# Kernel tuning notes

Hardware: AMD Instinct MI355X
Metric: run time of the kernel (lower is better)

## Reference

```python
import jax, jax.numpy as jnp
import numpy as np

B, S, NI, NQK, NV = 8, 2048, 1024, 128, 128

def setup_inputs() -> dict:
    key = jax.random.key(0)
    ks = jax.random.split(key, 7)
    sc_i = 1.0 / np.sqrt(NI)
    x = jax.random.normal(ks[0], (B, S, NI), dtype=jnp.float32)
    Wq = jax.random.uniform(ks[1], (NQK, NI), dtype=jnp.float32, minval=-sc_i, maxval=sc_i)
    bq = jax.random.uniform(ks[2], (NQK,), dtype=jnp.float32, minval=-sc_i, maxval=sc_i)
    Wk = jax.random.uniform(ks[3], (NQK, NI), dtype=jnp.float32, minval=-sc_i, maxval=sc_i)
    bk = jax.random.uniform(ks[4], (NQK,), dtype=jnp.float32, minval=-sc_i, maxval=sc_i)
    Wv = jax.random.uniform(ks[5], (NV, NI), dtype=jnp.float32, minval=-sc_i, maxval=sc_i)
    bv = jax.random.uniform(ks[6], (NV,), dtype=jnp.float32, minval=-sc_i, maxval=sc_i)
    return {"x": x, "Wq": Wq, "bq": bq, "Wk": Wk, "bk": bk, "Wv": Wv, "bv": bv}

def reference(x, Wq, bq, Wk, bk, Wv, bv):
    # torch nn.Linear: y = x @ W.T + b
    q = jnp.einsum('bsi,di->bsd', x, Wq) + bq  # [B,S,NQK]
    k = jnp.einsum('bsi,di->bsd', x, Wk) + bk  # [B,S,NQK]
    v = jnp.einsum('bsi,di->bsd', x, Wv) + bv  # [B,S,NV]
    # NOTE: original has no 1/sqrt(d) scaling
    Z = jnp.einsum('bqd,bkd->bqk', q, k)       # [B,S,S]
    Z = jax.nn.softmax(Z, axis=2)
    y = jnp.einsum('bqk,bkd->bqd', Z, v)       # [B,S,NV]
    return y
```

## Files before the change

### kernel.cpp

```cpp
#include <hip/hip_runtime.h>
#include <hip/hip_bf16.h>
#include <cstdint>

#define B_ 8
#define S_ 2048
#define NI_ 1024
#define D_ 128
#define M_ (B_ * S_)

typedef __attribute__((ext_vector_type(8))) short bf16x8;
typedef __attribute__((ext_vector_type(8))) unsigned short u16x8;
typedef __attribute__((ext_vector_type(4))) float f32x4;

__device__ __forceinline__ unsigned short f2bf(float f) {
    union { float f; uint32_t u; } v; v.f = f;
    uint32_t u = v.u;
    u += 0x7fff + ((u >> 16) & 1);
    return (unsigned short)(u >> 16);
}

__device__ __forceinline__ void gload16(const void* g, void* l) {
    __builtin_amdgcn_global_load_lds((const __attribute__((address_space(1))) void*)g,
                                     (__attribute__((address_space(3))) void*)l, 16, 0, 0);
}

__global__ __launch_bounds__(256) void k_pack_w(const float* __restrict__ Wq, const float* __restrict__ bq,
                                                const float* __restrict__ Wk, const float* __restrict__ bk,
                                                const float* __restrict__ Wv, const float* __restrict__ bv,
                                                unsigned short* __restrict__ wb, float* __restrict__ bias) {
    int t = blockIdx.x * 256 + threadIdx.x;
    int e = t * 8;
    const float* src; int off;
    if (e < 131072)      { src = Wq; off = e; }
    else if (e < 262144) { src = Wk; off = e - 131072; }
    else                 { src = Wv; off = e - 262144; }
    float4 a = *(const float4*)(src + off);
    float4 b = *(const float4*)(src + off + 4);
    u16x8 r;
    r[0] = f2bf(a.x); r[1] = f2bf(a.y); r[2] = f2bf(a.z); r[3] = f2bf(a.w);
    r[4] = f2bf(b.x); r[5] = f2bf(b.y); r[6] = f2bf(b.z); r[7] = f2bf(b.w);
    *(u16x8*)(wb + e) = r;
    if (t < 384)
        bias[t] = (t < 128) ? bq[t] : (t < 256) ? bk[t - 128] : bv[t - 256];
}

__global__ __launch_bounds__(256) void k_qkv(const float* __restrict__ x,
                                             const unsigned short* __restrict__ wb,
                                             const float* __restrict__ bias,
                                             unsigned short* __restrict__ q,
                                             unsigned short* __restrict__ kout,
                                             unsigned short* __restrict__ vT) {
    __shared__ __align__(16) unsigned short As[128 * 32];
    __shared__ __align__(16) unsigned short Bs[128 * 32];
    const int tid = threadIdx.x;
    const int m0 = blockIdx.x * 128;
    const int n0 = blockIdx.y * 128;
    const int l = tid & 63, w = tid >> 6;
    const int wr = w >> 1, wc = w & 1;
    const int lr = l & 15, lg = l >> 4;
    const int sr = tid >> 2;
    const int sc = (tid & 3) * 8;

    f32x4 acc[4][4] = {};

    for (int k0 = 0; k0 < NI_; k0 += 32) {
        gload16(wb + (long)(n0 + sr) * NI_ + k0 + sc,        Bs + tid * 8);
        gload16(wb + (long)(n0 + 64 + sr) * NI_ + k0 + sc,   Bs + 2048 + tid * 8);
        const float* xg0 = x + (long)(m0 + sr) * NI_ + k0 + sc;
        const float* xg1 = x + (long)(m0 + 64 + sr) * NI_ + k0 + sc;
        float4 a0 = *(const float4*)xg0, a1 = *(const float4*)(xg0 + 4);
        float4 a2 = *(const float4*)xg1, a3 = *(const float4*)(xg1 + 4);
        union { __hip_bfloat162 h[4]; u16x8 v; } r0, r1;
        r0.h[0] = __float22bfloat162_rn(make_float2(a0.x, a0.y));
        r0.h[1] = __float22bfloat162_rn(make_float2(a0.z, a0.w));
        r0.h[2] = __float22bfloat162_rn(make_float2(a1.x, a1.y));
        r0.h[3] = __float22bfloat162_rn(make_float2(a1.z, a1.w));
        r1.h[0] = __float22bfloat162_rn(make_float2(a2.x, a2.y));
        r1.h[1] = __float22bfloat162_rn(make_float2(a2.z, a2.w));
        r1.h[2] = __float22bfloat162_rn(make_float2(a3.x, a3.y));
        r1.h[3] = __float22bfloat162_rn(make_float2(a3.z, a3.w));
        *(u16x8*)(As + tid * 8) = r0.v;
        *(u16x8*)(As + 2048 + tid * 8) = r1.v;
        __syncthreads();
        bf16x8 a[4], b[4];
#pragma unroll
        for (int i = 0; i < 4; i++)
            a[i] = *(const bf16x8*)(As + (wr * 64 + i * 16 + lr) * 32 + lg * 8);
#pragma unroll
        for (int j = 0; j < 4; j++)
            b[j] = *(const bf16x8*)(Bs + (wc * 64 + j * 16 + lr) * 32 + lg * 8);
#pragma unroll
        for (int i = 0; i < 4; i++)
#pragma unroll
            for (int j = 0; j < 4; j++)
                acc[i][j] = __builtin_amdgcn_mfma_f32_16x16x32_bf16(a[i], b[j], acc[i][j], 0, 0, 0);
        __syncthreads();
    }

#pragma unroll
    for (int i = 0; i < 4; i++)
#pragma unroll
        for (int j = 0; j < 4; j++)
#pragma unroll
            for (int r = 0; r < 4; r++) {
                int row = m0 + wr * 64 + i * 16 + lg * 4 + r;
                int n = n0 + wc * 64 + j * 16 + lr;
                float val = acc[i][j][r] + bias[n];
                unsigned short bv16 = f2bf(val);
                if (n0 == 0)        q[(long)row * 128 + n] = bv16;
                else if (n0 == 128) kout[(long)row * 128 + (n - 128)] = bv16;
                else {
                    int bb = row >> 11, s = row & 2047, d = n - 256;
                    vT[((long)bb * 128 + d) * (long)S_ + s] = bv16;
                }
            }
}

#define SHIFT_ 16.0f
__global__ __launch_bounds__(256, 2) void k_attn(const unsigned short* __restrict__ q,
                                                 const unsigned short* __restrict__ kk,
                                                 const unsigned short* __restrict__ vT,
                                                 float* __restrict__ o_part,
                                                 float* __restrict__ L_part) {
    __shared__ __align__(16) unsigned short Kl[2 * 64 * 128];
    __shared__ __align__(16) unsigned short Vl[2 * 128 * 64];
    __shared__ __align__(16) unsigned short Plds[4 * 32 * 64];
    const int tid = threadIdx.x, l = tid & 63, w = tid >> 6;
    const int b = blockIdx.z, ks = blockIdx.y;
    const int q0 = blockIdx.x * 128 + w * 32;
    const int lr = l & 15, lg = l >> 4;
    const unsigned short* qB = q  + (long)b * S_ * 128;
    const unsigned short* kB = kk + (long)b * S_ * 128;
    const unsigned short* vB = vT + (long)b * 128 * S_;
    char* Pw = (char*)Plds + w * 4096;
    const int kv_base = ks * 512;
    const int lsw = (lr & 7) << 4;

    const int krow = tid >> 2, kcb = (tid & 3) * 64;
    const int vrow = tid >> 1, vcb = (tid & 1) * 64;
    const int kswz = (krow & 7) << 4, vswz = (vrow & 7) << 4;

    bf16x8 qf[2][4];
#pragma unroll
    for (int a = 0; a < 2; a++)
#pragma unroll
        for (int kc = 0; kc < 4; kc++)
            qf[a][kc] = *(const bf16x8*)(qB + (long)(q0 + a * 16 + lr) * 128 + kc * 32 + lg * 8);

    {
        const unsigned short* kg = kB + (long)(kv_base + krow) * 128 + (tid & 3) * 32;
        const unsigned short* vg = vB + (long)vrow * S_ + kv_base + (tid & 1) * 32;
        u16x8 k0v = *(const u16x8*)(kg),      k1v = *(const u16x8*)(kg + 8);
        u16x8 k2v = *(const u16x8*)(kg + 16), k3v = *(const u16x8*)(kg + 24);
        u16x8 v0v = *(const u16x8*)(vg),      v1v = *(const u16x8*)(vg + 8);
        u16x8 v2v = *(const u16x8*)(vg + 16), v3v = *(const u16x8*)(vg + 24);
        char* kd = (char*)Kl; char* vd = (char*)Vl;
        *(u16x8*)(kd + ((krow * 256 + kcb)      ^ kswz)) = k0v;
        *(u16x8*)(kd + ((krow * 256 + kcb + 16) ^ kswz)) = k1v;
        *(u16x8*)(kd + ((krow * 256 + kcb + 32) ^ kswz)) = k2v;
        *(u16x8*)(kd + ((krow * 256 + kcb + 48) ^ kswz)) = k3v;
        *(u16x8*)(vd + ((vrow * 128 + vcb)      ^ vswz)) = v0v;
        *(u16x8*)(vd + ((vrow * 128 + vcb + 16) ^ vswz)) = v1v;
        *(u16x8*)(vd + ((vrow * 128 + vcb + 32) ^ vswz)) = v2v;
        *(u16x8*)(vd + ((vrow * 128 + vcb + 48) ^ vswz)) = v3v;
    }
    __syncthreads();

    float psum[2][4] = {};
    f32x4 o[2][8] = {};
    int cur = 0;

    for (int t = 0; t < 8; t++) {
        u16x8 k0v, k1v, k2v, k3v, v0v, v1v, v2v, v3v;
        if (t < 7) {
            int kv = kv_base + (t + 1) * 64;
            const unsigned short* kg = kB + (long)(kv + krow) * 128 + (tid & 3) * 32;
            const unsigned short* vg = vB + (long)vrow * S_ + kv + (tid & 1) * 32;
            k0v = *(const u16x8*)(kg);      k1v = *(const u16x8*)(kg + 8);
            k2v = *(const u16x8*)(kg + 16); k3v = *(const u16x8*)(kg + 24);
            v0v = *(const u16x8*)(vg);      v1v = *(const u16x8*)(vg + 8);
            v2v = *(const u16x8*)(vg + 16); v3v = *(const u16x8*)(vg + 24);
        }

        const char* kd = (const char*)Kl + cur * 16384;
        const char* vd = (const char*)Vl + cur * 16384;

        f32x4 sa[2][4] = {};
#pragma unroll
        for (int j = 0; j < 4; j++) {
            bf16x8 kf[4];
#pragma unroll
            for (int kc = 0; kc < 4; kc++)
                kf[kc] = *(const bf16x8*)(kd + (((j * 16 + lr) * 256 + kc * 64 + lg * 16) ^ lsw));
#pragma unroll
            for (int a = 0; a < 2; a++)
#pragma unroll
                for (int kc = 0; kc < 4; kc++)
                    sa[a][j] = __builtin_amdgcn_mfma_f32_16x16x32_bf16(qf[a][kc], kf[kc], sa[a][j], 0, 0, 0);
        }

#pragma unroll
        for (int a = 0; a < 2; a++)
#pragma unroll
            for (int r = 0; r < 4; r++) {
                int row = a * 16 + lg * 4 + r;
#pragma unroll
                for (int j = 0; j < 4; j++) {
                    float pj = __expf(sa[a][j][r] - SHIFT_);
                    psum[a][r] += pj;
                    int bo = (row * 128 + (j * 16 + lr) * 2) ^ ((row & 7) << 4);
                    *(unsigned short*)(Pw + bo) = f2bf(pj);
                }
            }

        bf16x8 pa[2][2];
#pragma unroll
        for (int a = 0; a < 2; a++) {
            pa[a][0] = *(const bf16x8*)(Pw + (((a * 16 + lr) * 128 + lg * 16) ^ lsw));
            pa[a][1] = *(const bf16x8*)(Pw + (((a * 16 + lr) * 128 + 64 + lg * 16) ^ lsw));
        }

#pragma unroll
        for (int c = 0; c < 8; c++) {
            int dr = c * 16 + lr;
            bf16x8 vf0 = *(const bf16x8*)(vd + ((dr * 128 + lg * 16) ^ lsw));
            bf16x8 vf1 = *(const bf16x8*)(vd + ((dr * 128 + 64 + lg * 16) ^ lsw));
#pragma unroll
            for (int a = 0; a < 2; a++) {
                o[a][c] = __builtin_amdgcn_mfma_f32_16x16x32_bf16(pa[a][0], vf0, o[a][c], 0, 0, 0);
                o[a][c] = __builtin_amdgcn_mfma_f32_16x16x32_bf16(pa[a][1], vf1, o[a][c], 0, 0, 0);
            }
        }

        if (t < 7) {
            char* kdn = (char*)Kl + (cur ^ 1) * 16384;
            char* vdn = (char*)Vl + (cur ^ 1) * 16384;
            *(u16x8*)(kdn + ((krow * 256 + kcb)      ^ kswz)) = k0v;
            *(u16x8*)(kdn + ((krow * 256 + kcb + 16) ^ kswz)) = k1v;
            *(u16x8*)(kdn + ((krow * 256 + kcb + 32) ^ kswz)) = k2v;
            *(u16x8*)(kdn + ((krow * 256 + kcb + 48) ^ kswz)) = k3v;
            *(u16x8*)(vdn + ((vrow * 128 + vcb)      ^ vswz)) = v0v;
            *(u16x8*)(vdn + ((vrow * 128 + vcb + 16) ^ vswz)) = v1v;
            *(u16x8*)(vdn + ((vrow * 128 + vcb + 32) ^ vswz)) = v2v;
            *(u16x8*)(vdn + ((vrow * 128 + vcb + 48) ^ vswz)) = v3v;
        }
        __syncthreads();
        cur ^= 1;
    }

#pragma unroll
    for (int a = 0; a < 2; a++)
#pragma unroll
        for (int r = 0; r < 4; r++) {
            float ps = psum[a][r];
            ps += __shfl_xor(ps, 1);
            ps += __shfl_xor(ps, 2);
            ps += __shfl_xor(ps, 4);
            ps += __shfl_xor(ps, 8);
            if (lr == 0)
                L_part[((long)ks * B_ + b) * S_ + q0 + a * 16 + lg * 4 + r] = ps;
        }
#pragma unroll
    for (int a = 0; a < 2; a++)
#pragma unroll
        for (int c = 0; c < 8; c++)
#pragma unroll
            for (int r = 0; r < 4; r++) {
                int row = q0 + a * 16 + lg * 4 + r, col = c * 16 + lr;
                o_part[(((long)ks * B_ + b) * S_ + row) * 128 + col] = o[a][c][r];
            }
}

__global__ __launch_bounds__(256) void k_comb(const float* __restrict__ op,
                                              const float* __restrict__ Lp,
                                              float* __restrict__ out) {
    int t = blockIdx.x * 256 + threadIdx.x;
    int row = t >> 5;
    int c4 = (t & 31) * 4;
    float ax = 0.f, ay = 0.f, az = 0.f, aw = 0.f, Ls = 0.f;
#pragma unroll
    for (int ts = 0; ts < 4; ts++) {
        float4 v = *(const float4*)(op + (((long)ts * M_ + row) << 7) + c4);
        ax += v.x; ay += v.y; az += v.z; aw += v.w;
        Ls += Lp[(long)ts * M_ + row];
    }
    float inv = 1.f / Ls;
    float4 r; r.x = ax * inv; r.y = ay * inv; r.z = az * inv; r.w = aw * inv;
    *(float4*)(out + ((long)row << 7) + c4) = r;
}

extern "C" void kernel_launch(void* const* d_in, const int* in_sizes, int n_in,
                              void* d_out, int out_size, void* d_ws, size_t ws_size,
                              hipStream_t stream) {
    const float* x  = (const float*)d_in[0];
    const float* Wq = (const float*)d_in[1];
    const float* bq = (const float*)d_in[2];
    const float* Wk = (const float*)d_in[3];
    const float* bk = (const float*)d_in[4];
    const float* Wv = (const float*)d_in[5];
    const float* bv = (const float*)d_in[6];
    float* out = (float*)d_out;

    char* ws = (char*)d_ws;
    unsigned short* wb   = (unsigned short*)(ws + 33554432);
    float*          bias = (float*)(ws + 33554432 + 786432);
    unsigned short* qb   = (unsigned short*)(ws + 34344960);
    unsigned short* kb   = (unsigned short*)(ws + 38539264);
    unsigned short* vT   = (unsigned short*)(ws + 42733568);
    float* o_part = (float*)(ws);
    float* L_part = (float*)(ws + 46927872);

    k_pack_w<<<192, 256, 0, stream>>>(Wq, bq, Wk, bk, Wv, bv, wb, bias);
    k_qkv<<<dim3(128, 3), 256, 0, stream>>>(x, wb, bias, qb, kb, vT);
    k_attn<<<dim3(16, 4, 8), 256, 0, stream>>>(qb, kb, vT, o_part, L_part);
    k_comb<<<2048, 256, 0, stream>>>(o_part, L_part, out);
}
```

Measured before the change: 91.31 us.

## Double-buffer QKV projection GEMM and halve M tile to 64 rows

The QKV projection kernel now double-buffers its shared-memory tiles. The next K-slice of weights (async LDS load) and x (register prefetch) is issued before the MFMAs on the current slice. This removes one barrier per iteration and overlaps global loads with compute. The M tile is halved to 64 rows, doubling the grid to 768 blocks so more workgroups fill the CUs. The trade-off is that weight tiles are re-read twice as often and each block does less MFMA work per load.

New measurement: 78.31 us. 1.17x faster.

```diff
diff --git a/kernel.cpp b/kernel.cpp
--- a/kernel.cpp
+++ b/kernel.cpp
@@ -50,10 +50,10 @@
                                              unsigned short* __restrict__ q,
                                              unsigned short* __restrict__ kout,
                                              unsigned short* __restrict__ vT) {
-    __shared__ __align__(16) unsigned short As[128 * 32];
-    __shared__ __align__(16) unsigned short Bs[128 * 32];
+    __shared__ __align__(16) unsigned short As[2][64 * 32];
+    __shared__ __align__(16) unsigned short Bs[2][128 * 32];
     const int tid = threadIdx.x;
-    const int m0 = blockIdx.x * 128;
+    const int m0 = blockIdx.x * 64;
     const int n0 = blockIdx.y * 128;
     const int l = tid & 63, w = tid >> 6;
     const int wr = w >> 1, wc = w & 1;
@@ -61,49 +61,65 @@
     const int sr = tid >> 2;
     const int sc = (tid & 3) * 8;
 
-    f32x4 acc[4][4] = {};
-
-    for (int k0 = 0; k0 < NI_; k0 += 32) {
-        gload16(wb + (long)(n0 + sr) * NI_ + k0 + sc,        Bs + tid * 8);
-        gload16(wb + (long)(n0 + 64 + sr) * NI_ + k0 + sc,   Bs + 2048 + tid * 8);
-        const float* xg0 = x + (long)(m0 + sr) * NI_ + k0 + sc;
-        const float* xg1 = x + (long)(m0 + 64 + sr) * NI_ + k0 + sc;
-        float4 a0 = *(const float4*)xg0, a1 = *(const float4*)(xg0 + 4);
-        float4 a2 = *(const float4*)xg1, a3 = *(const float4*)(xg1 + 4);
-        union { __hip_bfloat162 h[4]; u16x8 v; } r0, r1;
+    f32x4 acc[2][4] = {};
+    float4 a0, a1;
+
+    a0 = *(const float4*)(x + (long)(m0 + sr) * NI_ + sc);
+    a1 = *(const float4*)(x + (long)(m0 + sr) * NI_ + sc + 4);
+    gload16(wb + (long)(n0 + sr) * NI_ + sc,      (unsigned short*)Bs[0] + tid * 8);
+    gload16(wb + (long)(n0 + 64 + sr) * NI_ + sc, (unsigned short*)Bs[0] + 2048 + tid * 8);
+    {
+        union { __hip_bfloat162 h[4]; u16x8 v; } r0;
         r0.h[0] = __float22bfloat162_rn(make_float2(a0.x, a0.y));
         r0.h[1] = __float22bfloat162_rn(make_float2(a0.z, a0.w));
         r0.h[2] = __float22bfloat162_rn(make_float2(a1.x, a1.y));
         r0.h[3] = __float22bfloat162_rn(make_float2(a1.z, a1.w));
-        r1.h[0] = __float22bfloat162_rn(make_float2(a2.x, a2.y));
-        r1.h[1] = __float22bfloat162_rn(make_float2(a2.z, a2.w));
-        r1.h[2] = __float22bfloat162_rn(make_float2(a3.x, a3.y));
-        r1.h[3] = __float22bfloat162_rn(make_float2(a3.z, a3.w));
-        *(u16x8*)(As + tid * 8) = r0.v;
-        *(u16x8*)(As + 2048 + tid * 8) = r1.v;
-        __syncthreads();
-        bf16x8 a[4], b[4];
-#pragma unroll
-        for (int i = 0; i < 4; i++)
-            a[i] = *(const bf16x8*)(As + (wr * 64 + i * 16 + lr) * 32 + lg * 8);
+        *(u16x8*)((unsigned short*)As[0] + tid * 8) = r0.v;
+    }
+    __syncthreads();
+
+    int cur = 0;
+    for (int k0 = 0; k0 < NI_; k0 += 32) {
+        bool more = (k0 + 32 < NI_);
+        if (more) {
+            gload16(wb + (long)(n0 + sr) * NI_ + k0 + 32 + sc,      (unsigned short*)Bs[cur ^ 1] + tid * 8);
+            gload16(wb + (long)(n0 + 64 + sr) * NI_ + k0 + 32 + sc, (unsigned short*)Bs[cur ^ 1] + 2048 + tid * 8);
+            a0 = *(const float4*)(x + (long)(m0 + sr) * NI_ + k0 + 32 + sc);
+            a1 = *(const float4*)(x + (long)(m0 + sr) * NI_ + k0 + 32 + sc + 4);
+        }
+
+        bf16x8 a[2], b[4];
+#pragma unroll
+        for (int i = 0; i < 2; i++)
+            a[i] = *(const bf16x8*)((unsigned short*)As[cur] + (wr * 32 + i * 16 + lr) * 32 + lg * 8);
 #pragma unroll
         for (int j = 0; j < 4; j++)
-            b[j] = *(const bf16x8*)(Bs + (wc * 64 + j * 16 + lr) * 32 + lg * 8);
-#pragma unroll
-        for (int i = 0; i < 4; i++)
+            b[j] = *(const bf16x8*)((unsigned short*)Bs[cur] + (wc * 64 + j * 16 + lr) * 32 + lg * 8);
+#pragma unroll
+        for (int i = 0; i < 2; i++)
 #pragma unroll
             for (int j = 0; j < 4; j++)
                 acc[i][j] = __builtin_amdgcn_mfma_f32_16x16x32_bf16(a[i], b[j], acc[i][j], 0, 0, 0);
+
+        if (more) {
+            union { __hip_bfloat162 h[4]; u16x8 v; } r0;
+            r0.h[0] = __float22bfloat162_rn(make_float2(a0.x, a0.y));
+            r0.h[1] = __float22bfloat162_rn(make_float2(a0.z, a0.w));
+            r0.h[2] = __float22bfloat162_rn(make_float2(a1.x, a1.y));
+            r0.h[3] = __float22bfloat162_rn(make_float2(a1.z, a1.w));
+            *(u16x8*)((unsigned short*)As[cur ^ 1] + tid * 8) = r0.v;
+        }
         __syncthreads();
-    }
-
-#pragma unroll
-    for (int i = 0; i < 4; i++)
+        cur ^= 1;
+    }
+
+#pragma unroll
+    for (int i = 0; i < 2; i++)
 #pragma unroll
         for (int j = 0; j < 4; j++)
 #pragma unroll
             for (int r = 0; r < 4; r++) {
-                int row = m0 + wr * 64 + i * 16 + lg * 4 + r;
+                int row = m0 + wr * 32 + i * 16 + lg * 4 + r;
                 int n = n0 + wc * 64 + j * 16 + lr;
                 float val = acc[i][j][r] + bias[n];
                 unsigned short bv16 = f2bf(val);
@@ -311,7 +327,7 @@
     float* L_part = (float*)(ws + 46927872);
 
     k_pack_w<<<192, 256, 0, stream>>>(Wq, bq, Wk, bk, Wv, bv, wb, bias);
-    k_qkv<<<dim3(128, 3), 256, 0, stream>>>(x, wb, bias, qb, kb, vT);
+    k_qkv<<<dim3(256, 3), 256, 0, stream>>>(x, wb, bias, qb, kb, vT);
     k_attn<<<dim3(16, 4, 8), 256, 0, stream>>>(qb, kb, vT, o_part, L_part);
     k_comb<<<2048, 256, 0, stream>>>(o_part, L_part, out);
 }
```

## Double-buffer LDS tiles in QKV projection GEMM to overlap loads with MFMA

Applied to the files above, without the earlier changes.

The QKV projection kernel now keeps two LDS buffers for the A and B tiles. It prefetches the next K-slice (global-to-LDS for weights, register loads for x) before running the MFMAs on the current slice. The fp32-to-bf16 conversion and the LDS write of the next A tile happen after the MFMAs, which removes one barrier per iteration. In exchange, LDS use doubles and register pressure rises, which may lower occupancy.

Result: faster. 85.36 us (-6.5%).

```diff
diff --git a/kernel.cpp b/kernel.cpp
--- a/kernel.cpp
+++ b/kernel.cpp
@@ -50,8 +50,8 @@
                                              unsigned short* __restrict__ q,
                                              unsigned short* __restrict__ kout,
                                              unsigned short* __restrict__ vT) {
-    __shared__ __align__(16) unsigned short As[128 * 32];
-    __shared__ __align__(16) unsigned short Bs[128 * 32];
+    __shared__ __align__(16) unsigned short As[2][128 * 32];
+    __shared__ __align__(16) unsigned short Bs[2][128 * 32];
     const int tid = threadIdx.x;
     const int m0 = blockIdx.x * 128;
     const int n0 = blockIdx.y * 128;
@@ -62,40 +62,61 @@
     const int sc = (tid & 3) * 8;
 
     f32x4 acc[4][4] = {};
-
+    float4 a0, a1, a2, a3;
+
+#define LOADA(k0off) do { \
+    const float* xg0 = x + (long)(m0 + sr) * NI_ + (k0off) + sc; \
+    const float* xg1 = x + (long)(m0 + 64 + sr) * NI_ + (k0off) + sc; \
+    a0 = *(const float4*)xg0; a1 = *(const float4*)(xg0 + 4); \
+    a2 = *(const float4*)xg1; a3 = *(const float4*)(xg1 + 4); } while (0)
+
+#define CVTWRITEA(buf) do { \
+    union { __hip_bfloat162 h[4]; u16x8 v; } r0, r1; \
+    r0.h[0] = __float22bfloat162_rn(make_float2(a0.x, a0.y)); \
+    r0.h[1] = __float22bfloat162_rn(make_float2(a0.z, a0.w)); \
+    r0.h[2] = __float22bfloat162_rn(make_float2(a1.x, a1.y)); \
+    r0.h[3] = __float22bfloat162_rn(make_float2(a1.z, a1.w)); \
+    r1.h[0] = __float22bfloat162_rn(make_float2(a2.x, a2.y)); \
+    r1.h[1] = __float22bfloat162_rn(make_float2(a2.z, a2.w)); \
+    r1.h[2] = __float22bfloat162_rn(make_float2(a3.x, a3.y)); \
+    r1.h[3] = __float22bfloat162_rn(make_float2(a3.z, a3.w)); \
+    *(u16x8*)((unsigned short*)As[buf] + tid * 8) = r0.v; \
+    *(u16x8*)((unsigned short*)As[buf] + 2048 + tid * 8) = r1.v; } while (0)
+
+    LOADA(0);
+    gload16(wb + (long)(n0 + sr) * NI_ + sc,      (unsigned short*)Bs[0] + tid * 8);
+    gload16(wb + (long)(n0 + 64 + sr) * NI_ + sc, (unsigned short*)Bs[0] + 2048 + tid * 8);
+    CVTWRITEA(0);
+    __syncthreads();
+
+    int cur = 0;
     for (int k0 = 0; k0 < NI_; k0 += 32) {
-        gload16(wb + (long)(n0 + sr) * NI_ + k0 + sc,        Bs + tid * 8);
-        gload16(wb + (long)(n0 + 64 + sr) * NI_ + k0 + sc,   Bs + 2048 + tid * 8);
-        const float* xg0 = x + (long)(m0 + sr) * NI_ + k0 + sc;
-        const float* xg1 = x + (long)(m0 + 64 + sr) * NI_ + k0 + sc;
-        float4 a0 = *(const float4*)xg0, a1 = *(const float4*)(xg0 + 4);
-        float4 a2 = *(const float4*)xg1, a3 = *(const float4*)(xg1 + 4);
-        union { __hip_bfloat162 h[4]; u16x8 v; } r0, r1;
-        r0.h[0] = __float22bfloat162_rn(make_float2(a0.x, a0.y));
-        r0.h[1] = __float22bfloat162_rn(make_float2(a0.z, a0.w));
-        r0.h[2] = __float22bfloat162_rn(make_float2(a1.x, a1.y));
-        r0.h[3] = __float22bfloat162_rn(make_float2(a1.z, a1.w));
-        r1.h[0] = __float22bfloat162_rn(make_float2(a2.x, a2.y));
-        r1.h[1] = __float22bfloat162_rn(make_float2(a2.z, a2.w));
-        r1.h[2] = __float22bfloat162_rn(make_float2(a3.x, a3.y));
-        r1.h[3] = __float22bfloat162_rn(make_float2(a3.z, a3.w));
-        *(u16x8*)(As + tid * 8) = r0.v;
-        *(u16x8*)(As + 2048 + tid * 8) = r1.v;
-        __syncthreads();
+        bool more = (k0 + 32 < NI_);
+        if (more) {
+            gload16(wb + (long)(n0 + sr) * NI_ + k0 + 32 + sc,      (unsigned short*)Bs[cur ^ 1] + tid * 8);
+            gload16(wb + (long)(n0 + 64 + sr) * NI_ + k0 + 32 + sc, (unsigned short*)Bs[cur ^ 1] + 2048 + tid * 8);
+            LOADA(k0 + 32);
+        }
+
         bf16x8 a[4], b[4];
 #pragma unroll
         for (int i = 0; i < 4; i++)
-            a[i] = *(const bf16x8*)(As + (wr * 64 + i * 16 + lr) * 32 + lg * 8);
+            a[i] = *(const bf16x8*)((unsigned short*)As[cur] + (wr * 64 + i * 16 + lr) * 32 + lg * 8);
 #pragma unroll
         for (int j = 0; j < 4; j++)
-            b[j] = *(const bf16x8*)(Bs + (wc * 64 + j * 16 + lr) * 32 + lg * 8);
+            b[j] = *(const bf16x8*)((unsigned short*)Bs[cur] + (wc * 64 + j * 16 + lr) * 32 + lg * 8);
 #pragma unroll
         for (int i = 0; i < 4; i++)
 #pragma unroll
             for (int j = 0; j < 4; j++)
                 acc[i][j] = __builtin_amdgcn_mfma_f32_16x16x32_bf16(a[i], b[j], acc[i][j], 0, 0, 0);
+
+        if (more) CVTWRITEA(cur ^ 1);
         __syncthreads();
+        cur ^= 1;
     }
+#undef LOADA
+#undef CVTWRITEA
 
 #pragma unroll
     for (int i = 0; i < 4; i++)
```
